# Optimization experiments

Measured on AMD Instinct MI355X. Metric: run time of the kernel, lower is better.

## Reference

```python
import jax, jax.numpy as jnp
import numpy as np

B = 64
A_DIM, T_DIM, V_DIM = 512, 1024, 512
H = 96
O1, O2, O3 = 6, 1, 3
HP1 = H + 1  # 97


def setup_inputs() -> dict:
    key = jax.random.key(0)
    ks = jax.random.split(key, 20)
    s = 0.02
    inp = {
        "audios": jax.random.normal(ks[0], (B, A_DIM), jnp.float32),
        "texts": jax.random.normal(ks[1], (B, T_DIM), jnp.float32),
        "videos": jax.random.normal(ks[2], (B, V_DIM), jnp.float32),
        # MLP encoders: Linear(in, hidden) + ReLU (dropout is identity at eval)
        "Wa": jax.random.normal(ks[3], (A_DIM, H), jnp.float32) * s,
        "ba": jnp.zeros((H,), jnp.float32),
        "Wt": jax.random.normal(ks[4], (T_DIM, H), jnp.float32) * s,
        "bt": jnp.zeros((H,), jnp.float32),
        "Wv": jax.random.normal(ks[5], (V_DIM, H), jnp.float32) * s,
        "bv": jnp.zeros((H,), jnp.float32),
        # post-fusion MLP
        "W1": jax.random.normal(ks[6], (HP1 * HP1 * HP1, H), jnp.float32) * s,
        "b1": jnp.zeros((H,), jnp.float32),
        "W2": jax.random.normal(ks[7], (H, H), jnp.float32) * s,
        "b2": jnp.zeros((H,), jnp.float32),
        # output heads
        "Wo1": jax.random.normal(ks[8], (H, O1), jnp.float32) * s,
        "bo1": jnp.zeros((O1,), jnp.float32),
        "Wo2": jax.random.normal(ks[9], (H, O2), jnp.float32) * s,
        "bo2": jnp.zeros((O2,), jnp.float32),
        "Wo3": jax.random.normal(ks[10], (H, O3), jnp.float32) * s,
        "bo3": jnp.zeros((O3,), jnp.float32),
    }
    return inp


def reference(audios, texts, videos, Wa, ba, Wt, bt, Wv, bv,
              W1, b1, W2, b2, Wo1, bo1, Wo2, bo2, Wo3, bo3):
    # encoders (eval mode: dropout = identity)
    ah = jax.nn.relu(audios @ Wa + ba)   # [B, H]
    th = jax.nn.relu(texts @ Wt + bt)    # [B, H]
    vh = jax.nn.relu(videos @ Wv + bv)   # [B, H]

    one = jnp.ones((ah.shape[0], 1), ah.dtype)
    a1 = jnp.concatenate([one, ah], axis=1)  # [B, H+1]
    v1 = jnp.concatenate([one, vh], axis=1)  # [B, H+1]
    t1 = jnp.concatenate([one, th], axis=1)  # [B, H+1]

    # trilinear outer product: bmm(a1[:, :, None], v1[:, None, :]) -> [B, A, V]
    # then bmm with t1 -> [B, A*V, T]; flatten order is (a, v, t)
    fusion = jnp.einsum('ba,bv,bt->bavt', a1, v1, t1).reshape(a1.shape[0], -1)

    y1 = jax.nn.relu(fusion @ W1 + b1)
    features = jax.nn.relu(y1 @ W2 + b2)

    emos_out = features @ Wo1 + bo1
    vals_out = features @ Wo2 + bo2
    sents_out = features @ Wo3 + bo3
    interloss = jnp.zeros((), jnp.float32)
    return (features, emos_out, vals_out, sents_out, interloss)
```

## Files before the change

kernel.cpp:

```cpp
#include <hip/hip_runtime.h>


typedef unsigned int u32;
typedef short frag8s __attribute__((ext_vector_type(8)));
typedef float f32x4 __attribute__((ext_vector_type(4)));

constexpr int G3     = 589;
constexpr int NRUN   = 9409;
constexpr int NRUNP  = 9412;
constexpr int NGROUP = 2353;
constexpr int RBLK   = 776;

constexpr int WS_A1T  = 0;
constexpr int WS_V1T  = WS_A1T + 98 * 64;
constexpr int WS_T1T  = WS_V1T + 98 * 64;
constexpr int WS_T1PK = WS_T1T + 98 * 64;
constexpr int WS_S    = WS_T1PK + 64 * 64;
constexpr int WS_WAT  = WS_S + NRUNP * 64;
constexpr int WS_WTT  = WS_WAT + 96 * 512;
constexpr int WS_WVT  = WS_WTT + 96 * 1024;
constexpr int WS_PART = WS_WVT + 96 * 512;
constexpr int WS_PART2= WS_PART + G3 * 6144;

__device__ __forceinline__ u32 bfrne(float x) {
    u32 u = __float_as_uint(x);
    return (u + 0x7FFFu + ((u >> 16) & 1u)) >> 16;
}
__device__ __forceinline__ float bflo(u32 p) { return __uint_as_float(p << 16); }
__device__ __forceinline__ float bfhi(u32 p) { return __uint_as_float(p & 0xFFFF0000u); }

__device__ __forceinline__ void async_cp16(float* lds, const float* g) {
    __builtin_amdgcn_global_load_lds((const __attribute__((address_space(1))) u32*)g,
                                     (__attribute__((address_space(3))) u32*)lds, 16, 0, 0);
}
__device__ __forceinline__ void async_cp4(float* lds, const float* g) {
    __builtin_amdgcn_global_load_lds((const __attribute__((address_space(1))) u32*)g,
                                     (__attribute__((address_space(3))) u32*)lds, 4, 0, 0);
}

__global__ void k0_transpose(const float* __restrict__ Wa, const float* __restrict__ Wt,
                             const float* __restrict__ Wv, float* __restrict__ ws) {
    int idx = blockIdx.x * 256 + threadIdx.x;
    if (idx < 49152) {
        int h = idx / 512, k = idx % 512;
        ws[WS_WAT + h * 512 + k] = Wa[k * 96 + h];
    } else if (idx < 147456) {
        int i = idx - 49152; int h = i / 1024, k = i % 1024;
        ws[WS_WTT + h * 1024 + k] = Wt[k * 96 + h];
    } else if (idx < 196608) {
        int i = idx - 147456; int h = i / 512, k = i % 512;
        ws[WS_WVT + h * 512 + k] = Wv[k * 96 + h];
    }
}

__global__ __launch_bounds__(256) void k1_enc(const float* __restrict__ audios,
                                              const float* __restrict__ texts,
                                              const float* __restrict__ videos,
                                              const float* __restrict__ ba,
                                              const float* __restrict__ bt,
                                              const float* __restrict__ bv,
                                              float* __restrict__ ws) {
    int wg = blockIdx.x, tid = threadIdx.x;
    int lane = tid & 63, wv = tid >> 6;
    if (wg == 288) {
        if (tid < 64) ws[WS_T1T + 97 * 64 + tid] = 0.0f;
        return;
    }
    int e = wg / 96, h = wg % 96;
    const float* in; const float* wt; float bias; int K; int outbase;
    if (e == 0)      { in = audios; wt = ws + WS_WAT + h * 512;  bias = ba[h]; K = 512;  outbase = WS_A1T; }
    else if (e == 1) { in = texts;  wt = ws + WS_WTT + h * 1024; bias = bt[h]; K = 1024; outbase = WS_T1T; }
    else             { in = videos; wt = ws + WS_WVT + h * 512;  bias = bv[h]; K = 512;  outbase = WS_V1T; }
    int nsweep = K >> 8;
    float4 wreg[4];
    for (int s = 0; s < nsweep; s++) wreg[s] = ((const float4*)wt)[s * 64 + lane];
    for (int pass = 0; pass < 16; pass++) {
        int b = pass * 4 + wv;
        float acc = 0.f;
        for (int s = 0; s < nsweep; s++) {
            float4 iv = ((const float4*)(in + b * K))[s * 64 + lane];
            acc += iv.x * wreg[s].x + iv.y * wreg[s].y + iv.z * wreg[s].z + iv.w * wreg[s].w;
        }
        for (int off = 32; off; off >>= 1) acc += __shfl_down(acc, off, 64);
        if (lane == 0) {
            float v = acc + bias;
            ws[outbase + (h + 1) * 64 + b] = v > 0.f ? v : 0.f;
        }
    }
    if (h == 0 && tid < 64) ws[outbase + tid] = 1.0f;
}

__global__ __launch_bounds__(256) void k2_s(float* __restrict__ ws) {
    int wg = blockIdx.x, tid = threadIdx.x;
    u32* t1pk = (u32*)ws + WS_T1PK;
    if (wg == 589) {
        for (int i = tid; i < 4096; i += 256) {
            int b = i >> 6, p = i & 63;
            u32 v = 0;
            if (p < 49) {
                float e0 = ws[WS_T1T + (2 * p) * 64 + b];
                float e1 = ws[WS_T1T + (2 * p + 1) * 64 + b];
                v = bfrne(e0) | (bfrne(e1) << 16);
            }
            t1pk[i] = v;
        }
        return;
    }
    for (int ii = 0; ii < 4; ii++) {
        int idx = wg * 1024 + ii * 256 + tid;
        if (idx >= NRUNP * 64) break;
        int run = idx >> 6, b = idx & 6 * 10 + 3;
        b = idx & 63;
        float s = 0.f;
        if (run < NRUN) {
            int i = run / 97, j = run % 97;
            s = ws[WS_A1T + i * 64 + b] * ws[WS_V1T + j * 64 + b];
        }
        ws[WS_S + idx] = s;
    }
}

__global__ __launch_bounds__(256) void k3_main(const float* __restrict__ W1,
                                               float* __restrict__ ws) {
    __shared__ float wtile[2][4 * RBLK];
    __shared__ u32   tpk[64 * 65];
    __shared__ float sl[2][4 * 64];

    int tid = threadIdx.x, lane = tid & 63, wv = tid >> 6;
    int id = blockIdx.x;
    const u32* t1pk_g = (const u32*)ws + WS_T1PK;
    const float* s_g = ws + WS_S;

    for (int i = tid; i < 2 * 4 * RBLK / 4; i += 256)
        ((float4*)wtile)[i] = make_float4(0.f, 0.f, 0.f, 0.f);
    for (int i = tid; i < 4096; i += 256) {
        int b = i >> 6, p = i & 63;
        tpk[b * 65 + p] = t1pk_g[i];
    }

    int glist[4]; int gcount = 0;
    for (int i2 = 0; i2 < 4; i2++) { int g = id + i2 * G3; if (g < NGROUP) glist[gcount++] = g; }

    f32x4 acc[6];
    for (int nt = 0; nt < 6; nt++) acc[nt] = f32x4{0.f, 0.f, 0.f, 0.f};

    auto stage_w = [&](int g, int koff, int buf) {
        int run = g * 4 + wv; if (run > 9408) run = 9408;
        if (koff < 96) {
            const float* gsrc = W1 + (size_t)(run * 97 + koff) * 96;
            float* ldst = &wtile[buf][wv * RBLK];
            for (int c = 0; c < 3; c++)
                async_cp16(ldst + c * 256, gsrc + c * 256 + lane * 4);
        } else {
            if (lane < 24)
                async_cp16(&wtile[buf][wv * RBLK], W1 + (size_t)(run * 97 + 96) * 96 + lane * 4);
        }
    };
    auto stage_s = [&](int g, int sb) {
        if (wv == 0) {
            for (int q2 = 0; q2 < 4; q2++) {
                int run = g * 4 + q2;
                async_cp4(&sl[sb][q2 * 64], s_g + run * 64 + lane);
            }
        }
    };

    stage_s(glist[0], 0);
    stage_w(glist[0], 0, 0);
    __syncthreads();

    int pw = 0, sb = 0;
    int b = (wv << 4) + (lane & 15);
    int q = lane >> 4;

    for (int gi = 0; gi < gcount; gi++) {
        int g = glist[gi];
        for (int step = 0; step < 13; step++) {
            int koff = step * 8;
            if (step < 12) stage_w(g, koff + 8, pw ^ 1);
            else if (gi + 1 < gcount) { stage_w(glist[gi + 1], 0, pw ^ 1); stage_s(glist[gi + 1], sb ^ 1); }

            float s = sl[sb][q * 64 + b];
            int pb = b * 65 + (koff >> 1);
            u32 ap[4];
#pragma unroll
            for (int r = 0; r < 4; r++) {
                u32 tp = tpk[pb + r];
                float fe = s * bflo(tp), fo = s * bfhi(tp);
                ap[r] = bfrne(fe) | (bfrne(fo) << 16);
            }
            union { u32 u[4]; frag8s f; } afr;
            afr.u[0] = ap[0]; afr.u[1] = ap[1]; afr.u[2] = ap[2]; afr.u[3] = ap[3];

            const float* wt0 = &wtile[pw][q * RBLK + (lane & 15)];
#pragma unroll
            for (int nt = 0; nt < 6; nt++) {
                union { u32 u[4]; frag8s f; } bfr;
#pragma unroll
                for (int r = 0; r < 4; r++) {
                    u32 w0 = __float_as_uint(wt0[(2 * r) * 96 + nt * 16]);
                    u32 w1 = __float_as_uint(wt0[(2 * r + 1) * 96 + nt * 16]);
                    bfr.u[r] = (w0 >> 16) | (w1 & 0xFFFF0000u);
                }
                acc[nt] = __builtin_amdgcn_mfma_f32_16x16x32_bf16(afr.f, bfr.f, acc[nt], 0, 0, 0);
            }
            __syncthreads();
            pw ^= 1;
        }
        sb ^= 1;
    }

    float* part = ws + WS_PART + (size_t)id * 6144;
#pragma unroll
    for (int nt = 0; nt < 6; nt++) {
#pragma unroll
        for (int r = 0; r < 4; r++) {
            int row = (wv << 4) + ((lane >> 4) << 2) + r;
            int col = nt * 16 + (lane & 15);
            part[row * 96 + col] = acc[nt][r];
        }
    }
}

__global__ __launch_bounds__(256) void k4a_reduce(float* __restrict__ ws) {
    int bid = blockIdx.x;
    int oc = bid % 24, wc = bid / 24;
    int o = oc * 256 + threadIdx.x;
    int w0 = wc * 74, w1 = w0 + 74; if (w1 > G3) w1 = G3;
    const float* part = ws + WS_PART + o;
    float a0 = 0.f, a1 = 0.f;
    int w = w0;
    for (; w + 2 <= w1; w += 2) {
        a0 += part[(size_t)w * 6144];
        a1 += part[(size_t)(w + 1) * 6144];
    }
    for (; w < w1; w++) a0 += part[(size_t)w * 6144];
    ws[WS_PART2 + (size_t)wc * 6144 + o] = a0 + a1;
}

__global__ __launch_bounds__(256) void k5_final(const float* __restrict__ b1,
                                                const float* __restrict__ W2, const float* __restrict__ b2,
                                                const float* __restrict__ Wo1, const float* __restrict__ bo1,
                                                const float* __restrict__ Wo2, const float* __restrict__ bo2,
                                                const float* __restrict__ Wo3, const float* __restrict__ bo3,
                                                const float* __restrict__ ws, float* __restrict__ out) {
    __shared__ float yl[8 * 96];
    __shared__ float w2l[96 * 97];
    __shared__ float fl[8 * 96];
    int tid = threadIdx.x;
    int row0 = blockIdx.x * 8;
    for (int i = tid; i < 768; i += 256) {
        int go = row0 * 96 + i;
        float acc = b1[i % 96];
#pragma unroll
        for (int w = 0; w < 8; w++) acc += ws[WS_PART2 + (size_t)w * 6144 + go];
        yl[i] = acc > 0.f ? acc : 0.f;
    }
    for (int i = tid; i < 9216; i += 256) { int k = i / 96, h = i % 96; w2l[k * 97 + h] = W2[i]; }
    __syncthreads();
    for (int i = tid; i < 768; i += 256) {
        int bb = i / 96, h = i % 96;
        float acc = b2[h];
#pragma unroll 8
        for (int k = 0; k < 96; k++) acc += yl[bb * 96 + k] * w2l[k * 97 + h];
        float f = acc > 0.f ? acc : 0.f;
        fl[i] = f; out[(row0 + bb) * 96 + h] = f;
    }
    __syncthreads();
    if (tid < 80) {
        if (tid < 48) {
            int lr = tid / 6, j = tid % 6;
            float acc = bo1[j];
            for (int k = 0; k < 96; k++) acc += fl[lr * 96 + k] * Wo1[k * 6 + j];
            out[6144 + (row0 + lr) * 6 + j] = acc;
        } else if (tid < 56) {
            int lr = tid - 48;
            float acc = bo2[0];
            for (int k = 0; k < 96; k++) acc += fl[lr * 96 + k] * Wo2[k];
            out[6528 + row0 + lr] = acc;
        } else {
            int t2 = tid - 56; int lr = t2 / 3, j = t2 % 3;
            float acc = bo3[j];
            for (int k = 0; k < 96; k++) acc += fl[lr * 96 + k] * Wo3[k * 3 + j];
            out[6592 + (row0 + lr) * 3 + j] = acc;
        }
    }
    if (blockIdx.x == 0 && tid == 0) out[6784] = 0.0f;
}

extern "C" void kernel_launch(void* const* d_in, const int* in_sizes, int n_in,
                              void* d_out, int out_size, void* d_ws, size_t ws_size,
                              hipStream_t stream) {
    (void)in_sizes; (void)n_in; (void)out_size; (void)ws_size;
    const float* audios = (const float*)d_in[0];
    const float* texts  = (const float*)d_in[1];
    const float* videos = (const float*)d_in[2];
    const float* Wa  = (const float*)d_in[3];
    const float* ba  = (const float*)d_in[4];
    const float* Wt  = (const float*)d_in[5];
    const float* bt  = (const float*)d_in[6];
    const float* Wv  = (const float*)d_in[7];
    const float* bv  = (const float*)d_in[8];
    const float* W1  = (const float*)d_in[9];
    const float* b1  = (const float*)d_in[10];
    const float* W2  = (const float*)d_in[11];
    const float* b2  = (const float*)d_in[12];
    const float* Wo1 = (const float*)d_in[13];
    const float* bo1 = (const float*)d_in[14];
    const float* Wo2 = (const float*)d_in[15];
    const float* bo2 = (const float*)d_in[16];
    const float* Wo3 = (const float*)d_in[17];
    const float* bo3 = (const float*)d_in[18];
    float* ws = (float*)d_ws;
    float* outp = (float*)d_out;

    k0_transpose<<<768, 256, 0, stream>>>(Wa, Wt, Wv, ws);
    k1_enc<<<289, 256, 0, stream>>>(audios, texts, videos, ba, bt, bv, ws);
    k2_s<<<590, 256, 0, stream>>>(ws);
    k3_main<<<G3, 256, 0, stream>>>(W1, ws);
    k4a_reduce<<<192, 256, 0, stream>>>(ws);
    k5_final<<<8, 256, 0, stream>>>(b1, W2, b2, Wo1, bo1, Wo2, bo2, Wo3, bo3, ws, outp);
}
```

Baseline: 595.2 us.

## Restructure main GEMM so each wave owns a run, using 32x32 MFMA and LDS reduction

The main fused-GEMM kernel now gives each wave its own run (k-slice of W1) and computes the full 64x96 output tile with 32x32x16 bf16 MFMAs. It stages 16 k-rows per step with explicit vmcnt waits in place of block-wide barriers every step, and holds the scale factors in registers. The four per-wave partial tiles are then summed through LDS before writing one partial per block. This is meant to cut per-step synchronisation and LDS traffic, and to get more MFMA work per fragment load. The cost is larger accumulators, which affect occupancy, plus an extra in-block reduction.

```diff
diff --git a/kernel.cpp b/kernel.cpp
--- a/kernel.cpp
+++ b/kernel.cpp
@@ -3,13 +3,12 @@
 
 typedef unsigned int u32;
 typedef short frag8s __attribute__((ext_vector_type(8)));
-typedef float f32x4 __attribute__((ext_vector_type(4)));
+typedef float f32x16 __attribute__((ext_vector_type(16)));
 
 constexpr int G3     = 589;
 constexpr int NRUN   = 9409;
 constexpr int NRUNP  = 9412;
 constexpr int NGROUP = 2353;
-constexpr int RBLK   = 776;
 
 constexpr int WS_A1T  = 0;
 constexpr int WS_V1T  = WS_A1T + 98 * 64;
@@ -32,10 +31,6 @@
 __device__ __forceinline__ void async_cp16(float* lds, const float* g) {
     __builtin_amdgcn_global_load_lds((const __attribute__((address_space(1))) u32*)g,
                                      (__attribute__((address_space(3))) u32*)lds, 16, 0, 0);
-}
-__device__ __forceinline__ void async_cp4(float* lds, const float* g) {
-    __builtin_amdgcn_global_load_lds((const __attribute__((address_space(1))) u32*)g,
-                                     (__attribute__((address_space(3))) u32*)lds, 4, 0, 0);
 }
 
 __global__ void k0_transpose(const float* __restrict__ Wa, const float* __restrict__ Wt,
@@ -109,8 +104,7 @@
     for (int ii = 0; ii < 4; ii++) {
         int idx = wg * 1024 + ii * 256 + tid;
         if (idx >= NRUNP * 64) break;
-        int run = idx >> 6, b = idx & 6 * 10 + 3;
-        b = idx & 63;
+        int run = idx >> 6, b = idx & 63;
         float s = 0.f;
         if (run < NRUN) {
             int i = run / 97, j = run % 97;
@@ -120,105 +114,143 @@
     }
 }
 
-__global__ __launch_bounds__(256) void k3_main(const float* __restrict__ W1,
-                                               float* __restrict__ ws) {
-    __shared__ float wtile[2][4 * RBLK];
-    __shared__ u32   tpk[64 * 65];
-    __shared__ float sl[2][4 * 64];
+__global__ __launch_bounds__(256, 2) void k3_main(const float* __restrict__ W1,
+                                                  float* __restrict__ ws) {
+    __shared__ float wtile[2][4][1536];
+    __shared__ u32   tpk[64 * 58];
 
     int tid = threadIdx.x, lane = tid & 63, wv = tid >> 6;
     int id = blockIdx.x;
+    int n = lane & 31, khalf = lane >> 5;
+
     const u32* t1pk_g = (const u32*)ws + WS_T1PK;
+    for (int i = tid; i < 3584; i += 256) {
+        int b = i / 56, p = i - b * 56;
+        tpk[b * 58 + p] = t1pk_g[b * 64 + p];
+    }
+
+    int glist[4]; int gcount = 0;
+    for (int t = 0; t < 4; t++) { int g = id + t * G3; if (g < NGROUP) glist[gcount++] = g; }
+
     const float* s_g = ws + WS_S;
-
-    for (int i = tid; i < 2 * 4 * RBLK / 4; i += 256)
-        ((float4*)wtile)[i] = make_float4(0.f, 0.f, 0.f, 0.f);
-    for (int i = tid; i < 4096; i += 256) {
-        int b = i >> 6, p = i & 63;
-        tpk[b * 65 + p] = t1pk_g[i];
-    }
-
-    int glist[4]; int gcount = 0;
-    for (int i2 = 0; i2 < 4; i2++) { int g = id + i2 * G3; if (g < NGROUP) glist[gcount++] = g; }
-
-    f32x4 acc[6];
-    for (int nt = 0; nt < 6; nt++) acc[nt] = f32x4{0.f, 0.f, 0.f, 0.f};
-
-    auto stage_w = [&](int g, int koff, int buf) {
-        int run = g * 4 + wv; if (run > 9408) run = 9408;
-        if (koff < 96) {
-            const float* gsrc = W1 + (size_t)(run * 97 + koff) * 96;
-            float* ldst = &wtile[buf][wv * RBLK];
-            for (int c = 0; c < 3; c++)
-                async_cp16(ldst + c * 256, gsrc + c * 256 + lane * 4);
-        } else {
-            if (lane < 24)
-                async_cp16(&wtile[buf][wv * RBLK], W1 + (size_t)(run * 97 + 96) * 96 + lane * 4);
-        }
+    float s0[4], s1[4];
+    for (int t = 0; t < gcount; t++) {
+        int rs = glist[t] * 4 + wv;
+        s0[t] = s_g[rs * 64 + n];
+        s1[t] = s_g[rs * 64 + 32 + n];
+    }
+
+    auto stage = [&](int runc, int k0, int buf) {
+        const float* g = W1 + ((size_t)runc * 97 + k0) * 96;
+        float* d = &wtile[buf][wv][0];
+        for (int c = 0; c < 6; c++) async_cp16(d + c * 256, g + c * 256 + lane * 4);
     };
-    auto stage_s = [&](int g, int sb) {
-        if (wv == 0) {
-            for (int q2 = 0; q2 < 4; q2++) {
-                int run = g * 4 + q2;
-                async_cp4(&sl[sb][q2 * 64], s_g + run * 64 + lane);
+    auto stage_tail = [&](int runc, int buf) {
+        const float* g = W1 + ((size_t)runc * 97 + 96) * 96;
+        if (lane < 24) async_cp16(&wtile[buf][wv][0], g + lane * 4);
+    };
+
+    f32x16 acc[2][3];
+    for (int mt = 0; mt < 2; mt++)
+        for (int nt = 0; nt < 3; nt++)
+            for (int e = 0; e < 16; e++) acc[mt][nt][e] = 0.f;
+
+    int runc0 = glist[0] * 4 + wv; if (runc0 > 9408) runc0 = 9408;
+    stage(runc0, 0, 0);
+    __syncthreads();
+
+    int pw = 0;
+    for (int gi = 0; gi < gcount; gi++) {
+        int runc = glist[gi] * 4 + wv; if (runc > 9408) runc = 9408;
+        float sa = s0[gi], sb = s1[gi];
+        for (int step = 0; step < 7; step++) {
+            if (step < 5) {
+                stage(runc, (step + 1) * 16, pw ^ 1);
+                asm volatile("s_waitcnt vmcnt(6) lgkmcnt(0)" ::: "memory");
+            } else if (step == 5) {
+                stage_tail(runc, pw ^ 1);
+                asm volatile("s_waitcnt vmcnt(1) lgkmcnt(0)" ::: "memory");
+            } else {
+                if (gi + 1 < gcount) {
+                    int rn = glist[gi + 1] * 4 + wv; if (rn > 9408) rn = 9408;
+                    stage(rn, 0, pw ^ 1);
+                    asm volatile("s_waitcnt vmcnt(6) lgkmcnt(0)" ::: "memory");
+                } else {
+                    asm volatile("s_waitcnt vmcnt(0) lgkmcnt(0)" ::: "memory");
+                }
             }
-        }
-    };
-
-    stage_s(glist[0], 0);
-    stage_w(glist[0], 0, 0);
-    __syncthreads();
-
-    int pw = 0, sb = 0;
-    int b = (wv << 4) + (lane & 15);
-    int q = lane >> 4;
-
-    for (int gi = 0; gi < gcount; gi++) {
-        int g = glist[gi];
-        for (int step = 0; step < 13; step++) {
-            int koff = step * 8;
-            if (step < 12) stage_w(g, koff + 8, pw ^ 1);
-            else if (gi + 1 < gcount) { stage_w(glist[gi + 1], 0, pw ^ 1); stage_s(glist[gi + 1], sb ^ 1); }
-
-            float s = sl[sb][q * 64 + b];
-            int pb = b * 65 + (koff >> 1);
-            u32 ap[4];
-#pragma unroll
-            for (int r = 0; r < 4; r++) {
-                u32 tp = tpk[pb + r];
-                float fe = s * bflo(tp), fo = s * bfhi(tp);
-                ap[r] = bfrne(fe) | (bfrne(fo) << 16);
+
+            const float* wt = &wtile[pw][wv][0] + n + khalf * 768;
+            union { u32 u[4]; frag8s f; } bfr[3];
+#pragma unroll
+            for (int nt = 0; nt < 3; nt++)
+#pragma unroll
+                for (int r = 0; r < 4; r++) {
+                    u32 w0 = __float_as_uint(wt[(2 * r) * 96 + nt * 32]);
+                    u32 w1 = __float_as_uint(wt[(2 * r + 1) * 96 + nt * 32]);
+                    bfr[nt].u[r] = (w0 >> 16) | (w1 & 0xFFFF0000u);
+                }
+            int pbase = step * 8 + khalf * 4;
+            union { u32 u[4]; frag8s f; } afr[2];
+#pragma unroll
+            for (int mt = 0; mt < 2; mt++) {
+                int b = n + 32 * mt;
+                const u32* tp = &tpk[b * 58 + pbase];
+                u32 t0 = tp[0], t1 = tp[1], t2 = tp[2], t3 = tp[3];
+                float sm = mt ? sb : sa;
+                u32 tt[4] = {t0, t1, t2, t3};
+#pragma unroll
+                for (int r = 0; r < 4; r++) {
+                    float fe = sm * bflo(tt[r]);
+                    float fo = sm * bfhi(tt[r]);
+                    afr[mt].u[r] = bfrne(fe) | (bfrne(fo) << 16);
+                }
             }
-            union { u32 u[4]; frag8s f; } afr;
-            afr.u[0] = ap[0]; afr.u[1] = ap[1]; afr.u[2] = ap[2]; afr.u[3] = ap[3];
-
-            const float* wt0 = &wtile[pw][q * RBLK + (lane & 15)];
-#pragma unroll
-            for (int nt = 0; nt < 6; nt++) {
-                union { u32 u[4]; frag8s f; } bfr;
-#pragma unroll
-                for (int r = 0; r < 4; r++) {
-                    u32 w0 = __float_as_uint(wt0[(2 * r) * 96 + nt * 16]);
-                    u32 w1 = __float_as_uint(wt0[(2 * r + 1) * 96 + nt * 16]);
-                    bfr.u[r] = (w0 >> 16) | (w1 & 0xFFFF0000u);
-                }
-                acc[nt] = __builtin_amdgcn_mfma_f32_16x16x32_bf16(afr.f, bfr.f, acc[nt], 0, 0, 0);
-            }
-            __syncthreads();
+#pragma unroll
+            for (int mt = 0; mt < 2; mt++)
+#pragma unroll
+                for (int nt = 0; nt < 3; nt++)
+                    acc[mt][nt] = __builtin_amdgcn_mfma_f32_32x32x16_bf16(
+                        afr[mt].f, bfr[nt].f, acc[mt][nt], 0, 0, 0);
             pw ^= 1;
         }
-        sb ^= 1;
-    }
-
+    }
+
+    __syncthreads();
+    float* red = &wtile[0][0][0];
+    if (wv >= 2) {
+        float* r = red + (size_t)(wv - 2) * 6144;
+#pragma unroll
+        for (int mt = 0; mt < 2; mt++)
+#pragma unroll
+            for (int nt = 0; nt < 3; nt++)
+#pragma unroll
+                for (int reg = 0; reg < 16; reg++) {
+                    int row = mt * 32 + (reg & 3) + 8 * (reg >> 2) + 4 * khalf;
+                    r[row * 96 + nt * 32 + n] = acc[mt][nt][reg];
+                }
+    }
+    __syncthreads();
+    if (wv < 2) {
+        float* r = red + (size_t)wv * 6144;
+#pragma unroll
+        for (int mt = 0; mt < 2; mt++)
+#pragma unroll
+            for (int nt = 0; nt < 3; nt++)
+#pragma unroll
+                for (int reg = 0; reg < 16; reg++) {
+                    int row = mt * 32 + (reg & 3) + 8 * (reg >> 2) + 4 * khalf;
+                    int idx = row * 96 + nt * 32 + n;
+                    r[idx] += acc[mt][nt][reg];
+                }
+    }
+    __syncthreads();
     float* part = ws + WS_PART + (size_t)id * 6144;
-#pragma unroll
-    for (int nt = 0; nt < 6; nt++) {
-#pragma unroll
-        for (int r = 0; r < 4; r++) {
-            int row = (wv << 4) + ((lane >> 4) << 2) + r;
-            int col = nt * 16 + (lane & 15);
-            part[row * 96 + col] = acc[nt][r];
-        }
+    for (int i = tid * 4; i < 6144; i += 1024) {
+        float4 a4 = *(const float4*)(red + i);
+        float4 b4 = *(const float4*)(red + 6144 + i);
+        float4 o; o.x = a4.x + b4.x; o.y = a4.y + b4.y; o.z = a4.z + b4.z; o.w = a4.w + b4.w;
+        *(float4*)(part + i) = o;
     }
 }
 
```

Result: no change. 603.1 us (+1.3%).
